# Performance work log

Measured on AMD Instinct MI355X. Metric: run time of the kernel, lower is better.

Reference implementation:

```python
import jax, jax.numpy as jnp
import numpy as np

VOCAB, EMB, CLASSES = 100000, 128, 1000
B, L = 16384, 200


def setup_inputs() -> dict:
    key = jax.random.key(0)
    k1, k2, k3, k4 = jax.random.split(key, 4)
    seq = jax.random.randint(k1, (B, L), 0, VOCAB, dtype=jnp.int64) if jax.config.jax_enable_x64 else jax.random.randint(k1, (B, L), 0, VOCAB).astype(jnp.int32)
    emb_table = jax.random.normal(k2, (VOCAB, EMB), dtype=jnp.float32) * 0.02
    fc_w = jax.random.normal(k3, (CLASSES, EMB), dtype=jnp.float32) * 0.02
    fc_b = jax.random.normal(k4, (CLASSES,), dtype=jnp.float32) * 0.02
    return {"seq": seq, "emb_table": emb_table, "fc_w": fc_w, "fc_b": fc_b}


def reference(seq, emb_table, fc_w, fc_b):
    # Masked embedding-bag (sum pool): tokens with id 0 are padding and excluded,
    # exactly matching the original nonzero-gather-sum loop.
    mask = (seq != 0).astype(emb_table.dtype)          # [B, L]
    gathered = emb_table[seq]                          # [B, L, E]
    pooled = jnp.einsum("ble,bl->be", gathered, mask)  # [B, E] sum over valid tokens
    return pooled @ fc_w.T + fc_b                      # [B, C]
```

## Files before the change

### kernel.cpp

```cpp
#include <hip/hip_runtime.h>

#define VOCAB   100000
#define EMB     128
#define CLASSES 1000
#define BATCH   16384
#define SEQLEN  200

typedef short bf16x8 __attribute__((ext_vector_type(8)));
typedef float f32x4  __attribute__((ext_vector_type(4)));

__device__ __forceinline__ unsigned short f32_to_bf16(float f) {
    unsigned int u = __builtin_bit_cast(unsigned int, f);
    u += 0x7fffu + ((u >> 16) & 1u);
    return (unsigned short)(u >> 16);
}
__device__ __forceinline__ float bf_lo(unsigned int p) { return __builtin_bit_cast(float, p << 16); }
__device__ __forceinline__ float bf_hi(unsigned int p) { return __builtin_bit_cast(float, p & 0xffff0000u); }
__device__ __forceinline__ float sb(unsigned int w, int sh) {
    return (float)(int)(signed char)((w >> sh) & 0xffu);
}

__global__ __launch_bounds__(256) void convert_emb_i8(const float* __restrict__ emb,
                                                      const float* __restrict__ fcw,
                                                      unsigned char* __restrict__ e8,
                                                      float* __restrict__ scl,
                                                      unsigned short* __restrict__ wb) {
    if (blockIdx.x < 6250) {
        const int row = blockIdx.x * 16 + (threadIdx.x >> 4);
        const int c8  = (threadIdx.x & 15) * 8;
        const float* r = emb + (long)row * EMB + c8;
        float4 v0 = *(const float4*)(r);
        float4 v1 = *(const float4*)(r + 4);
        float m = fmaxf(fmaxf(fmaxf(fabsf(v0.x), fabsf(v0.y)), fmaxf(fabsf(v0.z), fabsf(v0.w))),
                        fmaxf(fmaxf(fabsf(v1.x), fabsf(v1.y)), fmaxf(fabsf(v1.z), fabsf(v1.w))));
        m = fmaxf(m, __shfl_xor(m, 1));
        m = fmaxf(m, __shfl_xor(m, 2));
        m = fmaxf(m, __shfl_xor(m, 4));
        m = fmaxf(m, __shfl_xor(m, 8));
        const float inv = (m > 0.f) ? 127.0f / m : 0.f;
#define Q(x) ((int)fminf(fmaxf(__builtin_rintf((x) * inv), -127.f), 127.f))
        int q0 = Q(v0.x), q1 = Q(v0.y), q2 = Q(v0.z), q3 = Q(v0.w);
        int q4 = Q(v1.x), q5 = Q(v1.y), q6 = Q(v1.z), q7 = Q(v1.w);
#undef Q
        uint2 o;
        o.x = (unsigned int)(q0 & 255) | ((unsigned int)(q1 & 255) << 8) |
              ((unsigned int)(q2 & 255) << 16) | ((unsigned int)(q3 & 255) << 24);
        o.y = (unsigned int)(q4 & 255) | ((unsigned int)(q5 & 255) << 8) |
              ((unsigned int)(q6 & 255) << 16) | ((unsigned int)(q7 & 255) << 24);
        *(uint2*)(e8 + (long)row * EMB + c8) = o;
        if ((threadIdx.x & 15) == 0) scl[row] = m * (1.0f / 127.0f);
    } else {
        long i = (((long)blockIdx.x - 6250) * 256 + threadIdx.x) * 8;
        if (i >= (long)CLASSES * EMB) return;
        float4 v0 = *(const float4*)(fcw + i);
        float4 v1 = *(const float4*)(fcw + i + 4);
        uint4 o;
        o.x = (unsigned int)f32_to_bf16(v0.x) | ((unsigned int)f32_to_bf16(v0.y) << 16);
        o.y = (unsigned int)f32_to_bf16(v0.z) | ((unsigned int)f32_to_bf16(v0.w) << 16);
        o.z = (unsigned int)f32_to_bf16(v1.x) | ((unsigned int)f32_to_bf16(v1.y) << 16);
        o.w = (unsigned int)f32_to_bf16(v1.z) | ((unsigned int)f32_to_bf16(v1.w) << 16);
        *(uint4*)(wb + i) = o;
    }
}

__global__ __launch_bounds__(256) void convert_fcw(const float* __restrict__ fcw,
                                                   unsigned short* __restrict__ wb) {
    long i = ((long)blockIdx.x * 256 + threadIdx.x) * 8;
    if (i >= (long)CLASSES * EMB) return;
    float4 v0 = *(const float4*)(fcw + i);
    float4 v1 = *(const float4*)(fcw + i + 4);
    uint4 o;
    o.x = (unsigned int)f32_to_bf16(v0.x) | ((unsigned int)f32_to_bf16(v0.y) << 16);
    o.y = (unsigned int)f32_to_bf16(v0.z) | ((unsigned int)f32_to_bf16(v0.w) << 16);
    o.z = (unsigned int)f32_to_bf16(v1.x) | ((unsigned int)f32_to_bf16(v1.y) << 16);
    o.w = (unsigned int)f32_to_bf16(v1.z) | ((unsigned int)f32_to_bf16(v1.w) << 16);
    *(uint4*)(wb + i) = o;
}

__global__ __launch_bounds__(256) void bag_pool_i8(const int* __restrict__ seq,
                                                   const unsigned char* __restrict__ e8,
                                                   const float* __restrict__ scl,
                                                   unsigned short* __restrict__ pooled) {
    const int lane = threadIdx.x & 63;
    const int wid  = threadIdx.x >> 6;
    const int b    = blockIdx.x * 4 + wid;

    const int* srow = seq + (long)b * SEQLEN;
    int ids0 = srow[lane];
    int ids1 = srow[lane + 64];
    int ids2 = srow[lane + 128];
    int ids3 = (lane < 8) ? srow[lane + 192] : 0;

    const int quad = lane >> 4;
    const int dsub = (lane & 15) * 8;

    float a0 = 0.f, a1 = 0.f, a2 = 0.f, a3 = 0.f;
    float a4 = 0.f, a5 = 0.f, a6 = 0.f, a7 = 0.f;

#define ISSUE(IDS, G, T, U, S)                                                \
    T = __shfl((IDS), 4 * (G) + quad);                                        \
    U = *(const uint2*)(e8 + (long)T * EMB + dsub);                           \
    S = scl[T];

#define ACCUM(T, U, S)                                                        \
    {                                                                         \
        float ms = (T != 0) ? S : 0.0f;                                       \
        a0 += ms * sb(U.x, 0);  a1 += ms * sb(U.x, 8);                        \
        a2 += ms * sb(U.x, 16); a3 += ms * sb(U.x, 24);                       \
        a4 += ms * sb(U.y, 0);  a5 += ms * sb(U.y, 8);                        \
        a6 += ms * sb(U.y, 16); a7 += ms * sb(U.y, 24);                       \
    }

#define PIPE8(IDS, G0)                                                        \
    {                                                                         \
        int t0, t1, t2, t3, t4, t5, t6, t7;                                   \
        uint2 u0, u1, u2, u3, u4, u5, u6, u7;                                 \
        float s0, s1, s2, s3, s4, s5, s6, s7;                                 \
        ISSUE(IDS, (G0) + 0, t0, u0, s0)                                      \
        ISSUE(IDS, (G0) + 1, t1, u1, s1)                                      \
        ISSUE(IDS, (G0) + 2, t2, u2, s2)                                      \
        ISSUE(IDS, (G0) + 3, t3, u3, s3)                                      \
        ISSUE(IDS, (G0) + 4, t4, u4, s4)                                      \
        ISSUE(IDS, (G0) + 5, t5, u5, s5)                                      \
        ISSUE(IDS, (G0) + 6, t6, u6, s6)                                      \
        ISSUE(IDS, (G0) + 7, t7, u7, s7)                                      \
        ACCUM(t0, u0, s0) ACCUM(t1, u1, s1) ACCUM(t2, u2, s2) ACCUM(t3, u3, s3) \
        ACCUM(t4, u4, s4) ACCUM(t5, u5, s5) ACCUM(t6, u6, s6) ACCUM(t7, u7, s7) \
    }

    PIPE8(ids0, 0)
    PIPE8(ids0, 8)
    PIPE8(ids1, 0)
    PIPE8(ids1, 8)
    PIPE8(ids2, 0)
    PIPE8(ids2, 8)
    {
        int t0, t1;
        uint2 u0, u1;
        float s0, s1;
        ISSUE(ids3, 0, t0, u0, s0)
        ISSUE(ids3, 1, t1, u1, s1)
        ACCUM(t0, u0, s0) ACCUM(t1, u1, s1)
    }
#undef PIPE8
#undef ACCUM
#undef ISSUE

    a0 += __shfl_xor(a0, 16); a1 += __shfl_xor(a1, 16);
    a2 += __shfl_xor(a2, 16); a3 += __shfl_xor(a3, 16);
    a4 += __shfl_xor(a4, 16); a5 += __shfl_xor(a5, 16);
    a6 += __shfl_xor(a6, 16); a7 += __shfl_xor(a7, 16);
    a0 += __shfl_xor(a0, 32); a1 += __shfl_xor(a1, 32);
    a2 += __shfl_xor(a2, 32); a3 += __shfl_xor(a3, 32);
    a4 += __shfl_xor(a4, 32); a5 += __shfl_xor(a5, 32);
    a6 += __shfl_xor(a6, 32); a7 += __shfl_xor(a7, 32);

    if (lane < 16) {
        uint4 o;
        o.x = (unsigned int)f32_to_bf16(a0) | ((unsigned int)f32_to_bf16(a1) << 16);
        o.y = (unsigned int)f32_to_bf16(a2) | ((unsigned int)f32_to_bf16(a3) << 16);
        o.z = (unsigned int)f32_to_bf16(a4) | ((unsigned int)f32_to_bf16(a5) << 16);
        o.w = (unsigned int)f32_to_bf16(a6) | ((unsigned int)f32_to_bf16(a7) << 16);
        *(uint4*)(pooled + (long)b * EMB + dsub) = o;
    }
}

__global__ __launch_bounds__(256) void bag_pool_f32(const int* __restrict__ seq,
                                                    const float* __restrict__ emb,
                                                    unsigned short* __restrict__ pooled) {
    const int lane = threadIdx.x & 63;
    const int wid  = threadIdx.x >> 6;
    const int b    = blockIdx.x * 4 + wid;
    const int* srow = seq + (long)b * SEQLEN;
    int ids0 = srow[lane];
    int ids1 = srow[lane + 64];
    int ids2 = srow[lane + 128];
    int ids3 = (lane < 8) ? srow[lane + 192] : 0;
    const int half = lane >> 5;
    const int dsub = (lane & 31) * 4;
    float4 acc = {0.f, 0.f, 0.f, 0.f};
#define PAIR_BODY(IDS, Q)                                                   \
    {                                                                       \
        int tok = __shfl((IDS), 2 * (Q) + half);                            \
        if (tok != 0) {                                                     \
            float4 v = *(const float4*)(emb + (long)tok * EMB + dsub);      \
            acc.x += v.x; acc.y += v.y; acc.z += v.z; acc.w += v.w;         \
        }                                                                   \
    }
#pragma unroll 8
    for (int q = 0; q < 32; ++q) PAIR_BODY(ids0, q)
#pragma unroll 8
    for (int q = 0; q < 32; ++q) PAIR_BODY(ids1, q)
#pragma unroll 8
    for (int q = 0; q < 32; ++q) PAIR_BODY(ids2, q)
#pragma unroll
    for (int q = 0; q < 4; ++q)  PAIR_BODY(ids3, q)
#undef PAIR_BODY
    acc.x += __shfl_xor(acc.x, 32);
    acc.y += __shfl_xor(acc.y, 32);
    acc.z += __shfl_xor(acc.z, 32);
    acc.w += __shfl_xor(acc.w, 32);
    if (lane < 32) {
        uint2 o;
        o.x = (unsigned int)f32_to_bf16(acc.x) | ((unsigned int)f32_to_bf16(acc.y) << 16);
        o.y = (unsigned int)f32_to_bf16(acc.z) | ((unsigned int)f32_to_bf16(acc.w) << 16);
        *(uint2*)(pooled + (long)b * EMB + dsub) = o;
    }
}

__global__ __launch_bounds__(256) void bow_gemm(const unsigned short* __restrict__ pooled,
                                                const unsigned short* __restrict__ fcw,
                                                const float* __restrict__ fcb,
                                                float* __restrict__ out) {
    const int lane = threadIdx.x & 63;
    const int wid  = threadIdx.x >> 6;
    const int quad = lane >> 4;
    const int m0   = blockIdx.x * 64 + wid * 16;
    const int mrow = m0 + (lane & 15);
    const int koff = quad * 8;

    const unsigned short* ar = pooled + (long)mrow * EMB + koff;
    bf16x8 a0 = *(const bf16x8*)(ar + 0 * 32);
    bf16x8 a1 = *(const bf16x8*)(ar + 1 * 32);
    bf16x8 a2 = *(const bf16x8*)(ar + 2 * 32);
    bf16x8 a3 = *(const bf16x8*)(ar + 3 * 32);

    int ccur = (blockIdx.y * 21) * 16 + (lane & 15);
    const unsigned short* wr = fcw + (long)((ccur < CLASSES) ? ccur : 0) * EMB + koff;
    bf16x8 w0 = *(const bf16x8*)(wr + 0 * 32);
    bf16x8 w1 = *(const bf16x8*)(wr + 1 * 32);
    bf16x8 w2 = *(const bf16x8*)(wr + 2 * 32);
    bf16x8 w3 = *(const bf16x8*)(wr + 3 * 32);

#pragma unroll 1
    for (int i = 0; i < 21; ++i) {
        bf16x8 c0 = w0, c1 = w1, c2 = w2, c3 = w3;
        const int cc = ccur;
        if (i + 1 < 21) {
            ccur += 16;
            const unsigned short* wn = fcw + (long)((ccur < CLASSES) ? ccur : 0) * EMB + koff;
            w0 = *(const bf16x8*)(wn + 0 * 32);
            w1 = *(const bf16x8*)(wn + 1 * 32);
            w2 = *(const bf16x8*)(wn + 2 * 32);
            w3 = *(const bf16x8*)(wn + 3 * 32);
        }
        f32x4 acc = {0.f, 0.f, 0.f, 0.f};
        acc = __builtin_amdgcn_mfma_f32_16x16x32_bf16(a0, c0, acc, 0, 0, 0);
        acc = __builtin_amdgcn_mfma_f32_16x16x32_bf16(a1, c1, acc, 0, 0, 0);
        acc = __builtin_amdgcn_mfma_f32_16x16x32_bf16(a2, c2, acc, 0, 0, 0);
        acc = __builtin_amdgcn_mfma_f32_16x16x32_bf16(a3, c3, acc, 0, 0, 0);

        if (cc < CLASSES) {
            const float bias = fcb[cc];
            float* orow = out + (long)(m0 + quad * 4) * CLASSES + cc;
#pragma unroll
            for (int r = 0; r < 4; ++r)
                orow[(long)r * CLASSES] = acc[r] + bias;
        }
    }
}

extern "C" void kernel_launch(void* const* d_in, const int* in_sizes, int n_in,
                              void* d_out, int out_size, void* d_ws, size_t ws_size,
                              hipStream_t stream) {
    const int*   seq = (const int*)d_in[0];
    const float* emb = (const float*)d_in[1];
    const float* fcw = (const float*)d_in[2];
    const float* fcb = (const float*)d_in[3];
    float*       out = (float*)d_out;

    unsigned short* pooled   = (unsigned short*)d_ws;
    unsigned short* fcw_bf16 = pooled + (long)BATCH * EMB;
    float*          scl      = (float*)(fcw_bf16 + (long)CLASSES * EMB);
    unsigned char*  e8       = (unsigned char*)(scl + VOCAB);

    const size_t need = (size_t)BATCH * EMB * 2 + (size_t)CLASSES * EMB * 2 +
                        (size_t)VOCAB * 4 + (size_t)VOCAB * EMB;

    if (ws_size >= need) {
        convert_emb_i8<<<6313, 256, 0, stream>>>(emb, fcw, e8, scl, fcw_bf16);
        bag_pool_i8<<<BATCH / 4, 256, 0, stream>>>(seq, e8, scl, pooled);
    } else {
        convert_fcw<<<63, 256, 0, stream>>>(fcw, fcw_bf16);
        bag_pool_f32<<<BATCH / 4, 256, 0, stream>>>(seq, emb, pooled);
    }
    bow_gemm<<<dim3(BATCH / 64, 3), 256, 0, stream>>>(pooled, fcw_bf16, fcb, out);
}
```

Measured before the change: 188.4 us.

## Fuse int8 bag pooling with the bf16 MFMA classifier GEMM per 16-bag block

New measurement: 183.1 us. -2.8%, faster.

```diff
diff --git a/kernel.cpp b/kernel.cpp
--- a/kernel.cpp
+++ b/kernel.cpp
@@ -63,45 +63,24 @@
     }
 }
 
-__global__ __launch_bounds__(256) void convert_fcw(const float* __restrict__ fcw,
-                                                   unsigned short* __restrict__ wb) {
-    long i = ((long)blockIdx.x * 256 + threadIdx.x) * 8;
-    if (i >= (long)CLASSES * EMB) return;
-    float4 v0 = *(const float4*)(fcw + i);
-    float4 v1 = *(const float4*)(fcw + i + 4);
-    uint4 o;
-    o.x = (unsigned int)f32_to_bf16(v0.x) | ((unsigned int)f32_to_bf16(v0.y) << 16);
-    o.y = (unsigned int)f32_to_bf16(v0.z) | ((unsigned int)f32_to_bf16(v0.w) << 16);
-    o.z = (unsigned int)f32_to_bf16(v1.x) | ((unsigned int)f32_to_bf16(v1.y) << 16);
-    o.w = (unsigned int)f32_to_bf16(v1.z) | ((unsigned int)f32_to_bf16(v1.w) << 16);
-    *(uint4*)(wb + i) = o;
-}
-
-__global__ __launch_bounds__(256) void bag_pool_i8(const int* __restrict__ seq,
-                                                   const unsigned char* __restrict__ e8,
-                                                   const float* __restrict__ scl,
-                                                   unsigned short* __restrict__ pooled) {
+__global__ __launch_bounds__(256) void pool_gemm_i8(const int* __restrict__ seq,
+                                                    const unsigned char* __restrict__ e8,
+                                                    const float* __restrict__ scl,
+                                                    const unsigned short* __restrict__ fcw,
+                                                    const float* __restrict__ fcb,
+                                                    float* __restrict__ out) {
+    __shared__ unsigned short Asub[16][136];
+
     const int lane = threadIdx.x & 63;
     const int wid  = threadIdx.x >> 6;
-    const int b    = blockIdx.x * 4 + wid;
-
-    const int* srow = seq + (long)b * SEQLEN;
-    int ids0 = srow[lane];
-    int ids1 = srow[lane + 64];
-    int ids2 = srow[lane + 128];
-    int ids3 = (lane < 8) ? srow[lane + 192] : 0;
-
     const int quad = lane >> 4;
     const int dsub = (lane & 15) * 8;
-
-    float a0 = 0.f, a1 = 0.f, a2 = 0.f, a3 = 0.f;
-    float a4 = 0.f, a5 = 0.f, a6 = 0.f, a7 = 0.f;
+    const int bbase = blockIdx.x * 16;
 
 #define ISSUE(IDS, G, T, U, S)                                                \
     T = __shfl((IDS), 4 * (G) + quad);                                        \
     U = *(const uint2*)(e8 + (long)T * EMB + dsub);                           \
     S = scl[T];
-
 #define ACCUM(T, U, S)                                                        \
     {                                                                         \
         float ms = (T != 0) ? S : 0.0f;                                       \
@@ -110,7 +89,6 @@
         a4 += ms * sb(U.y, 0);  a5 += ms * sb(U.y, 8);                        \
         a6 += ms * sb(U.y, 16); a7 += ms * sb(U.y, 24);                       \
     }
-
 #define PIPE8(IDS, G0)                                                        \
     {                                                                         \
         int t0, t1, t2, t3, t4, t5, t6, t7;                                   \
@@ -128,41 +106,113 @@
         ACCUM(t4, u4, s4) ACCUM(t5, u5, s5) ACCUM(t6, u6, s6) ACCUM(t7, u7, s7) \
     }
 
-    PIPE8(ids0, 0)
-    PIPE8(ids0, 8)
-    PIPE8(ids1, 0)
-    PIPE8(ids1, 8)
-    PIPE8(ids2, 0)
-    PIPE8(ids2, 8)
-    {
-        int t0, t1;
-        uint2 u0, u1;
-        float s0, s1;
-        ISSUE(ids3, 0, t0, u0, s0)
-        ISSUE(ids3, 1, t1, u1, s1)
-        ACCUM(t0, u0, s0) ACCUM(t1, u1, s1)
+#pragma unroll 1
+    for (int j = 0; j < 4; ++j) {
+        const int bagLocal = wid * 4 + j;
+        const int* srow = seq + (long)(bbase + bagLocal) * SEQLEN;
+        int ids0 = srow[lane];
+        int ids1 = srow[lane + 64];
+        int ids2 = srow[lane + 128];
+        int ids3 = (lane < 8) ? srow[lane + 192] : 0;
+
+        float a0 = 0.f, a1 = 0.f, a2 = 0.f, a3 = 0.f;
+        float a4 = 0.f, a5 = 0.f, a6 = 0.f, a7 = 0.f;
+
+        PIPE8(ids0, 0)
+        PIPE8(ids0, 8)
+        PIPE8(ids1, 0)
+        PIPE8(ids1, 8)
+        PIPE8(ids2, 0)
+        PIPE8(ids2, 8)
+        {
+            int t0, t1;
+            uint2 u0, u1;
+            float s0, s1;
+            ISSUE(ids3, 0, t0, u0, s0)
+            ISSUE(ids3, 1, t1, u1, s1)
+            ACCUM(t0, u0, s0) ACCUM(t1, u1, s1)
+        }
+
+        a0 += __shfl_xor(a0, 16); a1 += __shfl_xor(a1, 16);
+        a2 += __shfl_xor(a2, 16); a3 += __shfl_xor(a3, 16);
+        a4 += __shfl_xor(a4, 16); a5 += __shfl_xor(a5, 16);
+        a6 += __shfl_xor(a6, 16); a7 += __shfl_xor(a7, 16);
+        a0 += __shfl_xor(a0, 32); a1 += __shfl_xor(a1, 32);
+        a2 += __shfl_xor(a2, 32); a3 += __shfl_xor(a3, 32);
+        a4 += __shfl_xor(a4, 32); a5 += __shfl_xor(a5, 32);
+        a6 += __shfl_xor(a6, 32); a7 += __shfl_xor(a7, 32);
+
+        if (lane < 16) {
+            uint4 o;
+            o.x = (unsigned int)f32_to_bf16(a0) | ((unsigned int)f32_to_bf16(a1) << 16);
+            o.y = (unsigned int)f32_to_bf16(a2) | ((unsigned int)f32_to_bf16(a3) << 16);
+            o.z = (unsigned int)f32_to_bf16(a4) | ((unsigned int)f32_to_bf16(a5) << 16);
+            o.w = (unsigned int)f32_to_bf16(a6) | ((unsigned int)f32_to_bf16(a7) << 16);
+            *(uint4*)(&Asub[bagLocal][dsub]) = o;
+        }
     }
 #undef PIPE8
 #undef ACCUM
 #undef ISSUE
 
-    a0 += __shfl_xor(a0, 16); a1 += __shfl_xor(a1, 16);
-    a2 += __shfl_xor(a2, 16); a3 += __shfl_xor(a3, 16);
-    a4 += __shfl_xor(a4, 16); a5 += __shfl_xor(a5, 16);
-    a6 += __shfl_xor(a6, 16); a7 += __shfl_xor(a7, 16);
-    a0 += __shfl_xor(a0, 32); a1 += __shfl_xor(a1, 32);
-    a2 += __shfl_xor(a2, 32); a3 += __shfl_xor(a3, 32);
-    a4 += __shfl_xor(a4, 32); a5 += __shfl_xor(a5, 32);
-    a6 += __shfl_xor(a6, 32); a7 += __shfl_xor(a7, 32);
-
-    if (lane < 16) {
-        uint4 o;
-        o.x = (unsigned int)f32_to_bf16(a0) | ((unsigned int)f32_to_bf16(a1) << 16);
-        o.y = (unsigned int)f32_to_bf16(a2) | ((unsigned int)f32_to_bf16(a3) << 16);
-        o.z = (unsigned int)f32_to_bf16(a4) | ((unsigned int)f32_to_bf16(a5) << 16);
-        o.w = (unsigned int)f32_to_bf16(a6) | ((unsigned int)f32_to_bf16(a7) << 16);
-        *(uint4*)(pooled + (long)b * EMB + dsub) = o;
-    }
+    __syncthreads();
+
+    const int arow = lane & 15;
+    bf16x8 A0 = *(const bf16x8*)(&Asub[arow][quad * 8 + 0]);
+    bf16x8 A1 = *(const bf16x8*)(&Asub[arow][quad * 8 + 32]);
+    bf16x8 A2 = *(const bf16x8*)(&Asub[arow][quad * 8 + 64]);
+    bf16x8 A3 = *(const bf16x8*)(&Asub[arow][quad * 8 + 96]);
+
+    const int koff = quad * 8;
+    int t = wid;
+    int cc = t * 16 + (lane & 15);
+    const unsigned short* wr = fcw + (long)((cc < CLASSES) ? cc : 0) * EMB + koff;
+    bf16x8 w0 = *(const bf16x8*)(wr + 0 * 32);
+    bf16x8 w1 = *(const bf16x8*)(wr + 1 * 32);
+    bf16x8 w2 = *(const bf16x8*)(wr + 2 * 32);
+    bf16x8 w3 = *(const bf16x8*)(wr + 3 * 32);
+
+#pragma unroll 1
+    while (t < 63) {
+        bf16x8 c0 = w0, c1 = w1, c2 = w2, c3 = w3;
+        const int ccNow = cc;
+        t += 4;
+        if (t < 63) {
+            cc = t * 16 + (lane & 15);
+            const unsigned short* wn = fcw + (long)((cc < CLASSES) ? cc : 0) * EMB + koff;
+            w0 = *(const bf16x8*)(wn + 0 * 32);
+            w1 = *(const bf16x8*)(wn + 1 * 32);
+            w2 = *(const bf16x8*)(wn + 2 * 32);
+            w3 = *(const bf16x8*)(wn + 3 * 32);
+        }
+        f32x4 acc = {0.f, 0.f, 0.f, 0.f};
+        acc = __builtin_amdgcn_mfma_f32_16x16x32_bf16(A0, c0, acc, 0, 0, 0);
+        acc = __builtin_amdgcn_mfma_f32_16x16x32_bf16(A1, c1, acc, 0, 0, 0);
+        acc = __builtin_amdgcn_mfma_f32_16x16x32_bf16(A2, c2, acc, 0, 0, 0);
+        acc = __builtin_amdgcn_mfma_f32_16x16x32_bf16(A3, c3, acc, 0, 0, 0);
+
+        if (ccNow < CLASSES) {
+            const float bias = fcb[ccNow];
+            float* orow = out + (long)(bbase + quad * 4) * CLASSES + ccNow;
+#pragma unroll
+            for (int r = 0; r < 4; ++r)
+                orow[(long)r * CLASSES] = acc[r] + bias;
+        }
+    }
+}
+
+__global__ __launch_bounds__(256) void convert_fcw(const float* __restrict__ fcw,
+                                                   unsigned short* __restrict__ wb) {
+    long i = ((long)blockIdx.x * 256 + threadIdx.x) * 8;
+    if (i >= (long)CLASSES * EMB) return;
+    float4 v0 = *(const float4*)(fcw + i);
+    float4 v1 = *(const float4*)(fcw + i + 4);
+    uint4 o;
+    o.x = (unsigned int)f32_to_bf16(v0.x) | ((unsigned int)f32_to_bf16(v0.y) << 16);
+    o.y = (unsigned int)f32_to_bf16(v0.z) | ((unsigned int)f32_to_bf16(v0.w) << 16);
+    o.z = (unsigned int)f32_to_bf16(v1.x) | ((unsigned int)f32_to_bf16(v1.y) << 16);
+    o.w = (unsigned int)f32_to_bf16(v1.z) | ((unsigned int)f32_to_bf16(v1.w) << 16);
+    *(uint4*)(wb + i) = o;
 }
 
 __global__ __launch_bounds__(256) void bag_pool_f32(const int* __restrict__ seq,
@@ -269,20 +319,20 @@
     const float* fcb = (const float*)d_in[3];
     float*       out = (float*)d_out;
 
-    unsigned short* pooled   = (unsigned short*)d_ws;
-    unsigned short* fcw_bf16 = pooled + (long)BATCH * EMB;
-    float*          scl      = (float*)(fcw_bf16 + (long)CLASSES * EMB);
+    float*          scl      = (float*)d_ws;
     unsigned char*  e8       = (unsigned char*)(scl + VOCAB);
-
-    const size_t need = (size_t)BATCH * EMB * 2 + (size_t)CLASSES * EMB * 2 +
-                        (size_t)VOCAB * 4 + (size_t)VOCAB * EMB;
+    unsigned short* fcw_bf16 = (unsigned short*)(e8 + (long)VOCAB * EMB);
+
+    const size_t need = (size_t)VOCAB * 4 + (size_t)VOCAB * EMB + (size_t)CLASSES * EMB * 2;
 
     if (ws_size >= need) {
         convert_emb_i8<<<6313, 256, 0, stream>>>(emb, fcw, e8, scl, fcw_bf16);
-        bag_pool_i8<<<BATCH / 4, 256, 0, stream>>>(seq, e8, scl, pooled);
+        pool_gemm_i8<<<BATCH / 16, 256, 0, stream>>>(seq, e8, scl, fcw_bf16, fcb, out);
     } else {
-        convert_fcw<<<63, 256, 0, stream>>>(fcw, fcw_bf16);
+        unsigned short* pooled  = (unsigned short*)d_ws;
+        unsigned short* fcw_bf  = pooled + (long)BATCH * EMB;
+        convert_fcw<<<63, 256, 0, stream>>>(fcw, fcw_bf);
         bag_pool_f32<<<BATCH / 4, 256, 0, stream>>>(seq, emb, pooled);
-    }
-    bow_gemm<<<dim3(BATCH / 64, 3), 256, 0, stream>>>(pooled, fcw_bf16, fcb, out);
-}
+        bow_gemm<<<dim3(BATCH / 64, 3), 256, 0, stream>>>(pooled, fcw_bf, fcb, out);
+    }
+}
```
